# Kernel optimization log

Hardware: AMD Instinct MI355X
Metric: run time of the kernel (lower is better)

## Reference

```python
import jax, jax.numpy as jnp
import numpy as np

NX, NY, D, K = 20000, 50000, 64, 8
NUM_BATCHES = 2


def _knn_np(px, py, bx, by, k):
    # Batched exact kNN via chunked squared-distance + argpartition (mirrors torch_cluster.knn under no_grad).
    pp = (px * px).sum(1)
    idx = np.empty((py.shape[0], k), np.int32)
    chunk = 4096
    for s in range(0, py.shape[0], chunk):
        q = py[s:s + chunk]
        d = (q * q).sum(1)[:, None] + pp[None, :] - 2.0 * (q @ px.T)
        d = np.where(by[s:s + chunk, None] == bx[None, :], d, np.inf)
        idx[s:s + chunk] = np.argpartition(d, k, axis=1)[:, :k].astype(np.int32)
    return idx


def setup_inputs() -> dict:
    rng = np.random.default_rng(0)
    pos_x = (rng.random((NX, 3)) * 10.0).astype(np.float32)
    pos_y = (rng.random((NY, 3)) * 10.0).astype(np.float32)
    bx = np.repeat(np.arange(NUM_BATCHES), NX // NUM_BATCHES).astype(np.int32)
    by = np.repeat(np.arange(NUM_BATCHES), NY // NUM_BATCHES).astype(np.int32)
    x_idx = _knn_np(pos_x, pos_y, bx, by, K).reshape(-1)            # [NY*K]
    y_idx = np.repeat(np.arange(NY, dtype=np.int32), K)             # [NY*K]

    key = jax.random.key(0)
    ks = jax.random.split(key, 6)

    def lin(k, fi, fo):
        return jax.random.normal(k, (fi, fo), jnp.float32) / np.sqrt(fi).astype(np.float32)

    return {
        "x": jax.random.normal(ks[0], (NX, D), jnp.float32),
        "pos_x": jnp.asarray(pos_x),
        "pos_y": jnp.asarray(pos_y),
        "x_idx": jnp.asarray(x_idx),
        "y_idx": jnp.asarray(y_idx),
        # ResnetBlockFC 1: size_in=D+3, size_h=D, size_out=D (shortcut linear, no bias)
        "W0a": lin(ks[1], D + 3, D), "b0a": jnp.zeros((D,), jnp.float32),
        "W1a": lin(ks[2], D, D),     "b1a": jnp.zeros((D,), jnp.float32),
        "Wsa": lin(ks[3], D + 3, D),
        # ResnetBlockFC 2: size_in=size_h=size_out=D (identity shortcut)
        "W0b": lin(ks[4], D, D),     "b0b": jnp.zeros((D,), jnp.float32),
        "W1b": lin(ks[5], D, D),     "b1b": jnp.zeros((D,), jnp.float32),
    }


def reference(x, pos_x, pos_y, x_idx, y_idx, W0a, b0a, W1a, b1a, Wsa, W0b, b0b, W1b, b1b):
    # gather + positional diff (diff computed under no_grad in the original)
    diff = jax.lax.stop_gradient(pos_x[x_idx] - pos_y[y_idx])        # [E, 3]
    h = jnp.concatenate([x[x_idx], diff], axis=1)                    # [E, D+3]
    # ResnetBlockFC 1: out = shortcut(h) + fc1(relu(fc0(relu(h))))
    net = jax.nn.relu(h) @ W0a + b0a
    dx = jax.nn.relu(net) @ W1a + b1a
    h = h @ Wsa + dx                                                 # [E, D]
    # ResnetBlockFC 2 (identity shortcut)
    net = jax.nn.relu(h) @ W0b + b0b
    h = h + jax.nn.relu(net) @ W1b + b1b                             # [E, D]
    # scatter-max back to query points (every query has exactly K edges)
    out = jax.ops.segment_max(h, y_idx, num_segments=NY)             # [NY, D]
    return out
```

## Files before the change

### kernel.cpp

```cpp
#include <hip/hip_runtime.h>


typedef _Float16 f16x8 __attribute__((ext_vector_type(8)));
typedef float    f32x4 __attribute__((ext_vector_type(4)));

constexpr int NROWS   = 50000 * 8;
constexpr int NPAIRS  = NROWS / 32;
constexpr int NFRAG   = 48;
constexpr int TSTRIDE = 72;
constexpr int BW      = 8;

static __device__ __forceinline__ void xpose_relu(const f32x4* acc, const float* bb,
                                                  _Float16* tbuf, int q, int n0,
                                                  f16x8* af) {
    __threadfence_block();
#pragma unroll
    for (int t = 0; t < 4; ++t)
#pragma unroll
        for (int r = 0; r < 4; ++r) {
            float v = acc[t][r] + bb[t];
            tbuf[(q * 4 + r) * TSTRIDE + t * 16 + n0] = (_Float16)(v > 0.0f ? v : 0.0f);
        }
    __threadfence_block();
#pragma unroll
    for (int s = 0; s < 2; ++s)
        af[s] = *(const f16x8*)&tbuf[n0 * TSTRIDE + s * 32 + q * 8];
}

__global__ __launch_bounds__(512, 4)
void pointnet_fused(const float* __restrict__ x,
                    const float* __restrict__ pos_x,
                    const float* __restrict__ pos_y,
                    const int*   __restrict__ x_idx,
                    const float* __restrict__ W0a, const float* __restrict__ b0a,
                    const float* __restrict__ W1a, const float* __restrict__ b1a,
                    const float* __restrict__ Wsa,
                    const float* __restrict__ W0b, const float* __restrict__ b0b,
                    const float* __restrict__ W1b, const float* __restrict__ b1b,
                    float* __restrict__ out)
{
    __shared__ __align__(16) _Float16 bfrag[NFRAG * 64 * 8];
    __shared__ __align__(16) _Float16 trans[BW][16 * TSTRIDE];
    __shared__ float bias_lds[4 * 64];

    const int tid = threadIdx.x;

    for (int p = tid; p < NFRAG * 64; p += 512) {
        const int f = p >> 6;
        const int l = p & 63;
        const float* W; int krows, fl;
        if (f < 12)      { W = W0a; krows = 67; fl = f; }
        else if (f < 20) { W = W1a; krows = 64; fl = f - 12; }
        else if (f < 32) { W = Wsa; krows = 67; fl = f - 20; }
        else if (f < 40) { W = W0b; krows = 64; fl = f - 32; }
        else             { W = W1b; krows = 64; fl = f - 40; }
        const int s = fl >> 2, t = fl & 3;
        const int n = t * 16 + (l & 15);
        const int kbase = s * 32 + (l >> 4) * 8;
        f16x8 v;
#pragma unroll
        for (int j = 0; j < 8; ++j) {
            const int k = kbase + j;
            v[j] = (_Float16)((k < krows) ? W[k * 64 + n] : 0.0f);
        }
        *(f16x8*)&bfrag[p * 8] = v;
    }
    if (tid < 256) {
        const int L = tid >> 6, i = tid & 63;
        const float* b = (L == 0) ? b0a : (L == 1) ? b1a : (L == 2) ? b0b : b1b;
        bias_lds[tid] = b[i];
    }
    __syncthreads();

    const int lane = tid & 63;
    const int wv   = tid >> 6;
    const int n0   = lane & 15;
    const int q    = lane >> 4;

    _Float16* tbuf = trans[wv];
    const int gwave  = blockIdx.x * BW + wv;
    const int nwaves = gridDim.x * BW;

    for (int pr = gwave; pr < NPAIRS; pr += nwaves) {
        f16x8 hn[2][3];
#pragma unroll
        for (int u = 0; u < 2; ++u) {
            const int row = pr * 32 + u * 16 + n0;
            const int xi  = x_idx[row];
            const float* xp = x + (long)xi * 64;
#pragma unroll
            for (int s = 0; s < 2; ++s) {
                const float4* src = (const float4*)(xp + s * 32 + q * 8);
                float4 v0 = src[0], v1 = src[1];
                float vals[8] = {v0.x, v0.y, v0.z, v0.w, v1.x, v1.y, v1.z, v1.w};
#pragma unroll
                for (int j = 0; j < 8; ++j)
                    hn[u][s][j] = (_Float16)vals[j];
            }
            f16x8 z = {};
            hn[u][2] = z;
            if (q == 0) {
                const int yi = row >> 3;
#pragma unroll
                for (int j = 0; j < 3; ++j)
                    hn[u][2][j] = (_Float16)(pos_x[xi * 3 + j] - pos_y[yi * 3 + j]);
            }
        }

        f32x4 A2[2][4];
#pragma unroll
        for (int u = 0; u < 2; ++u)
#pragma unroll
            for (int t = 0; t < 4; ++t)
                A2[u][t] = (f32x4){0.f, 0.f, 0.f, 0.f};
#pragma unroll
        for (int s = 0; s < 3; ++s)
#pragma unroll
            for (int t = 0; t < 4; ++t) {
                f16x8 b = *(const f16x8*)&bfrag[((20 + s * 4 + t) * 64 + lane) * 8];
                A2[0][t] = __builtin_amdgcn_mfma_f32_16x16x32_f16(hn[0][s], b, A2[0][t], 0, 0, 0);
                A2[1][t] = __builtin_amdgcn_mfma_f32_16x16x32_f16(hn[1][s], b, A2[1][t], 0, 0, 0);
            }

#pragma unroll
        for (int u = 0; u < 2; ++u)
#pragma unroll
            for (int s = 0; s < 3; ++s)
#pragma unroll
                for (int j = 0; j < 8; ++j) {
                    _Float16 v = hn[u][s][j];
                    hn[u][s][j] = v > (_Float16)0 ? v : (_Float16)0;
                }

        f32x4 A1[2][4];
#pragma unroll
        for (int u = 0; u < 2; ++u)
#pragma unroll
            for (int t = 0; t < 4; ++t)
                A1[u][t] = (f32x4){0.f, 0.f, 0.f, 0.f};
#pragma unroll
        for (int s = 0; s < 3; ++s)
#pragma unroll
            for (int t = 0; t < 4; ++t) {
                f16x8 b = *(const f16x8*)&bfrag[((s * 4 + t) * 64 + lane) * 8];
                A1[0][t] = __builtin_amdgcn_mfma_f32_16x16x32_f16(hn[0][s], b, A1[0][t], 0, 0, 0);
                A1[1][t] = __builtin_amdgcn_mfma_f32_16x16x32_f16(hn[1][s], b, A1[1][t], 0, 0, 0);
            }

        float bb[4];
#pragma unroll
        for (int t = 0; t < 4; ++t) bb[t] = bias_lds[0 * 64 + t * 16 + n0];
        f16x8 a2[2][2];
        xpose_relu(A1[0], bb, tbuf, q, n0, a2[0]);
        xpose_relu(A1[1], bb, tbuf, q, n0, a2[1]);
#pragma unroll
        for (int s = 0; s < 2; ++s)
#pragma unroll
            for (int t = 0; t < 4; ++t) {
                f16x8 b = *(const f16x8*)&bfrag[((12 + s * 4 + t) * 64 + lane) * 8];
                A2[0][t] = __builtin_amdgcn_mfma_f32_16x16x32_f16(a2[0][s], b, A2[0][t], 0, 0, 0);
                A2[1][t] = __builtin_amdgcn_mfma_f32_16x16x32_f16(a2[1][s], b, A2[1][t], 0, 0, 0);
            }

#pragma unroll
        for (int t = 0; t < 4; ++t) bb[t] = bias_lds[1 * 64 + t * 16 + n0];
#pragma unroll
        for (int u = 0; u < 2; ++u)
#pragma unroll
            for (int t = 0; t < 4; ++t)
#pragma unroll
                for (int r = 0; r < 4; ++r)
                    A2[u][t][r] += bb[t];
        const float bz[4] = {0.f, 0.f, 0.f, 0.f};
        f16x8 a4[2][2];
        xpose_relu(A2[0], bz, tbuf, q, n0, a4[0]);
        xpose_relu(A2[1], bz, tbuf, q, n0, a4[1]);

        f32x4 A3[2][4];
#pragma unroll
        for (int u = 0; u < 2; ++u)
#pragma unroll
            for (int t = 0; t < 4; ++t)
                A3[u][t] = (f32x4){0.f, 0.f, 0.f, 0.f};
#pragma unroll
        for (int s = 0; s < 2; ++s)
#pragma unroll
            for (int t = 0; t < 4; ++t) {
                f16x8 b = *(const f16x8*)&bfrag[((32 + s * 4 + t) * 64 + lane) * 8];
                A3[0][t] = __builtin_amdgcn_mfma_f32_16x16x32_f16(a4[0][s], b, A3[0][t], 0, 0, 0);
                A3[1][t] = __builtin_amdgcn_mfma_f32_16x16x32_f16(a4[1][s], b, A3[1][t], 0, 0, 0);
            }

#pragma unroll
        for (int t = 0; t < 4; ++t) bb[t] = bias_lds[2 * 64 + t * 16 + n0];
        f16x8 a5[2][2];
        xpose_relu(A3[0], bb, tbuf, q, n0, a5[0]);
        xpose_relu(A3[1], bb, tbuf, q, n0, a5[1]);

#pragma unroll
        for (int t = 0; t < 4; ++t) bb[t] = bias_lds[3 * 64 + t * 16 + n0];
#pragma unroll
        for (int u = 0; u < 2; ++u)
#pragma unroll
            for (int t = 0; t < 4; ++t)
#pragma unroll
                for (int r = 0; r < 4; ++r)
                    A2[u][t][r] += bb[t];
#pragma unroll
        for (int s = 0; s < 2; ++s)
#pragma unroll
            for (int t = 0; t < 4; ++t) {
                f16x8 b = *(const f16x8*)&bfrag[((40 + s * 4 + t) * 64 + lane) * 8];
                A2[0][t] = __builtin_amdgcn_mfma_f32_16x16x32_f16(a5[0][s], b, A2[0][t], 0, 0, 0);
                A2[1][t] = __builtin_amdgcn_mfma_f32_16x16x32_f16(a5[1][s], b, A2[1][t], 0, 0, 0);
            }

#pragma unroll
        for (int u = 0; u < 2; ++u)
#pragma unroll
            for (int t = 0; t < 4; ++t) {
                float pm = fmaxf(fmaxf(A2[u][t][0], A2[u][t][1]),
                                 fmaxf(A2[u][t][2], A2[u][t][3]));
                pm = fmaxf(pm, __shfl_xor(pm, 16, 64));
                if ((q & 1) == 0) {
                    const int y = pr * 4 + u * 2 + (q >> 1);
                    out[(long)y * 64 + t * 16 + n0] = pm;
                }
            }
    }
}

extern "C" void kernel_launch(void* const* d_in, const int* in_sizes, int n_in,
                              void* d_out, int out_size, void* d_ws, size_t ws_size,
                              hipStream_t stream) {
    (void)in_sizes; (void)n_in; (void)d_ws; (void)ws_size; (void)out_size;
    pointnet_fused<<<512, 512, 0, stream>>>(
        (const float*)d_in[0],
        (const float*)d_in[1],
        (const float*)d_in[2],
        (const int*)  d_in[3],
        (const float*)d_in[5],  (const float*)d_in[6],
        (const float*)d_in[7],  (const float*)d_in[8],
        (const float*)d_in[9],
        (const float*)d_in[10], (const float*)d_in[11],
        (const float*)d_in[12], (const float*)d_in[13],
        (float*)d_out);
}
```

Baseline: 126.1 us.

## Precast x to fp16, precompute position diffs, and software-prefetch next gather

Adds two small pre-kernels that convert x to fp16 and compute the fp16 positional differences per edge into workspace. The fused kernel then gathers half-size rows and software-pipelines the loads, fetching the next pair's features and the index after that one while the current pair computes. This is meant to cut gather bandwidth and hide the latency of dependent index-then-row loads. The cost is two extra launches, a workspace round-trip for the diff buffer, and more live registers, which may hurt occupancy.

```diff
diff --git a/kernel.cpp b/kernel.cpp
--- a/kernel.cpp
+++ b/kernel.cpp
@@ -2,13 +2,40 @@
 
 
 typedef _Float16 f16x8 __attribute__((ext_vector_type(8)));
+typedef _Float16 f16x4 __attribute__((ext_vector_type(4)));
 typedef float    f32x4 __attribute__((ext_vector_type(4)));
 
+constexpr int NX      = 20000;
 constexpr int NROWS   = 50000 * 8;
 constexpr int NPAIRS  = NROWS / 32;
 constexpr int NFRAG   = 48;
 constexpr int TSTRIDE = 72;
 constexpr int BW      = 8;
+constexpr size_t X16_BYTES = (size_t)NX * 64 * 2;
+
+__global__ void prep_x(const float* __restrict__ x, _Float16* __restrict__ x16) {
+    const int i = blockIdx.x * blockDim.x + threadIdx.x;
+    if (i < NX * 16) {
+        float4 v = ((const float4*)x)[i];
+        f16x4 o = {(_Float16)v.x, (_Float16)v.y, (_Float16)v.z, (_Float16)v.w};
+        *(f16x4*)(x16 + (size_t)i * 4) = o;
+    }
+}
+
+__global__ void prep_diff(const int* __restrict__ x_idx,
+                          const float* __restrict__ px, const float* __restrict__ py,
+                          _Float16* __restrict__ d16) {
+    const int r = blockIdx.x * blockDim.x + threadIdx.x;
+    if (r < NROWS) {
+        const int xi = x_idx[r];
+        const int yi = r >> 3;
+        f16x4 o = {(_Float16)(px[xi * 3 + 0] - py[yi * 3 + 0]),
+                   (_Float16)(px[xi * 3 + 1] - py[yi * 3 + 1]),
+                   (_Float16)(px[xi * 3 + 2] - py[yi * 3 + 2]),
+                   (_Float16)0};
+        *(f16x4*)(d16 + (size_t)r * 4) = o;
+    }
+}
 
 static __device__ __forceinline__ void xpose_relu(const f32x4* acc, const float* bb,
                                                   _Float16* tbuf, int q, int n0,
@@ -28,9 +55,8 @@
 }
 
 __global__ __launch_bounds__(512, 4)
-void pointnet_fused(const float* __restrict__ x,
-                    const float* __restrict__ pos_x,
-                    const float* __restrict__ pos_y,
+void pointnet_fused(const _Float16* __restrict__ x16,
+                    const _Float16* __restrict__ d16,
                     const int*   __restrict__ x_idx,
                     const float* __restrict__ W0a, const float* __restrict__ b0a,
                     const float* __restrict__ W1a, const float* __restrict__ b1a,
@@ -80,31 +106,57 @@
     _Float16* tbuf = trans[wv];
     const int gwave  = blockIdx.x * BW + wv;
     const int nwaves = gridDim.x * BW;
+    const int last   = ((NPAIRS - 1 - gwave) / nwaves) * nwaves + gwave;
+
+    f16x8 cra[2][2];
+    f16x4 crd[2];
+    int   xin[2];
+
+#pragma unroll
+    for (int u = 0; u < 2; ++u) {
+        const int row = gwave * 32 + u * 16 + n0;
+        const int xi  = x_idx[row];
+        const _Float16* xp = x16 + (long)xi * 64 + q * 8;
+        cra[u][0] = *(const f16x8*)(xp);
+        cra[u][1] = *(const f16x8*)(xp + 32);
+        crd[u] = (f16x4){0, 0, 0, 0};
+        if (q == 0) crd[u] = *(const f16x4*)(d16 + (long)row * 4);
+    }
+    {
+        const int prn = (gwave + nwaves <= last) ? gwave + nwaves : last;
+#pragma unroll
+        for (int u = 0; u < 2; ++u)
+            xin[u] = x_idx[prn * 32 + u * 16 + n0];
+    }
 
     for (int pr = gwave; pr < NPAIRS; pr += nwaves) {
         f16x8 hn[2][3];
 #pragma unroll
         for (int u = 0; u < 2; ++u) {
-            const int row = pr * 32 + u * 16 + n0;
-            const int xi  = x_idx[row];
-            const float* xp = x + (long)xi * 64;
-#pragma unroll
-            for (int s = 0; s < 2; ++s) {
-                const float4* src = (const float4*)(xp + s * 32 + q * 8);
-                float4 v0 = src[0], v1 = src[1];
-                float vals[8] = {v0.x, v0.y, v0.z, v0.w, v1.x, v1.y, v1.z, v1.w};
-#pragma unroll
-                for (int j = 0; j < 8; ++j)
-                    hn[u][s][j] = (_Float16)vals[j];
-            }
+            hn[u][0] = cra[u][0];
+            hn[u][1] = cra[u][1];
             f16x8 z = {};
             hn[u][2] = z;
             if (q == 0) {
-                const int yi = row >> 3;
-#pragma unroll
-                for (int j = 0; j < 3; ++j)
-                    hn[u][2][j] = (_Float16)(pos_x[xi * 3 + j] - pos_y[yi * 3 + j]);
-            }
+                hn[u][2][0] = crd[u][0];
+                hn[u][2][1] = crd[u][1];
+                hn[u][2][2] = crd[u][2];
+            }
+        }
+
+        {
+            const int prn = (pr + nwaves <= last) ? pr + nwaves : last;
+#pragma unroll
+            for (int u = 0; u < 2; ++u) {
+                const _Float16* xp = x16 + (long)xin[u] * 64 + q * 8;
+                cra[u][0] = *(const f16x8*)(xp);
+                cra[u][1] = *(const f16x8*)(xp + 32);
+                if (q == 0) crd[u] = *(const f16x4*)(d16 + (long)(prn * 32 + u * 16 + n0) * 4);
+            }
+            const int prn2 = (prn + nwaves <= last) ? prn + nwaves : last;
+#pragma unroll
+            for (int u = 0; u < 2; ++u)
+                xin[u] = x_idx[prn2 * 32 + u * 16 + n0];
         }
 
         f32x4 A2[2][4];
@@ -233,11 +285,16 @@
 extern "C" void kernel_launch(void* const* d_in, const int* in_sizes, int n_in,
                               void* d_out, int out_size, void* d_ws, size_t ws_size,
                               hipStream_t stream) {
-    (void)in_sizes; (void)n_in; (void)d_ws; (void)ws_size; (void)out_size;
+    (void)in_sizes; (void)n_in; (void)ws_size; (void)out_size;
+    _Float16* x16 = (_Float16*)d_ws;
+    _Float16* d16 = (_Float16*)((char*)d_ws + X16_BYTES);
+
+    prep_x<<<(NX * 16 + 255) / 256, 256, 0, stream>>>((const float*)d_in[0], x16);
+    prep_diff<<<(NROWS + 255) / 256, 256, 0, stream>>>(
+        (const int*)d_in[3], (const float*)d_in[1], (const float*)d_in[2], d16);
+
     pointnet_fused<<<512, 512, 0, stream>>>(
-        (const float*)d_in[0],
-        (const float*)d_in[1],
-        (const float*)d_in[2],
+        x16, d16,
         (const int*)  d_in[3],
         (const float*)d_in[5],  (const float*)d_in[6],
         (const float*)d_in[7],  (const float*)d_in[8],
```

New measurement: 134.8 us. 1.07x slower.

## Pre-convert x to fp16 and process single 16-row tiles with more waves

Applied to the files above, without the earlier changes.

Adds a prep kernel that converts x to fp16 in workspace so the gather loads half the bytes per edge row. The main kernel now handles one 16-row tile per wave iteration instead of two, cutting register pressure. It raises the block to 12 waves with a higher occupancy hint to keep more waves resident. The cost is an extra kernel launch plus a full pass over x, and less instruction-level parallelism per wave.

```diff
diff --git a/kernel.cpp b/kernel.cpp
--- a/kernel.cpp
+++ b/kernel.cpp
@@ -2,13 +2,25 @@
 
 
 typedef _Float16 f16x8 __attribute__((ext_vector_type(8)));
+typedef _Float16 f16x4 __attribute__((ext_vector_type(4)));
 typedef float    f32x4 __attribute__((ext_vector_type(4)));
 
+constexpr int NX      = 20000;
 constexpr int NROWS   = 50000 * 8;
-constexpr int NPAIRS  = NROWS / 32;
+constexpr int NTILES  = NROWS / 16;
 constexpr int NFRAG   = 48;
 constexpr int TSTRIDE = 72;
-constexpr int BW      = 8;
+constexpr int BW      = 12;
+constexpr int BLOCK   = 64 * BW;
+
+__global__ void prep_x(const float* __restrict__ x, _Float16* __restrict__ x16) {
+    const int i = blockIdx.x * blockDim.x + threadIdx.x;
+    if (i < NX * 16) {
+        float4 v = ((const float4*)x)[i];
+        f16x4 o = {(_Float16)v.x, (_Float16)v.y, (_Float16)v.z, (_Float16)v.w};
+        *(f16x4*)(x16 + (size_t)i * 4) = o;
+    }
+}
 
 static __device__ __forceinline__ void xpose_relu(const f32x4* acc, const float* bb,
                                                   _Float16* tbuf, int q, int n0,
@@ -27,8 +39,8 @@
         af[s] = *(const f16x8*)&tbuf[n0 * TSTRIDE + s * 32 + q * 8];
 }
 
-__global__ __launch_bounds__(512, 4)
-void pointnet_fused(const float* __restrict__ x,
+__global__ __launch_bounds__(BLOCK, 6)
+void pointnet_fused(const _Float16* __restrict__ x16,
                     const float* __restrict__ pos_x,
                     const float* __restrict__ pos_y,
                     const int*   __restrict__ x_idx,
@@ -45,7 +57,7 @@
 
     const int tid = threadIdx.x;
 
-    for (int p = tid; p < NFRAG * 64; p += 512) {
+    for (int p = tid; p < NFRAG * 64; p += BLOCK) {
         const int f = p >> 6;
         const int l = p & 63;
         const float* W; int krows, fl;
@@ -81,161 +93,135 @@
     const int gwave  = blockIdx.x * BW + wv;
     const int nwaves = gridDim.x * BW;
 
-    for (int pr = gwave; pr < NPAIRS; pr += nwaves) {
-        f16x8 hn[2][3];
-#pragma unroll
-        for (int u = 0; u < 2; ++u) {
-            const int row = pr * 32 + u * 16 + n0;
-            const int xi  = x_idx[row];
-            const float* xp = x + (long)xi * 64;
-#pragma unroll
-            for (int s = 0; s < 2; ++s) {
-                const float4* src = (const float4*)(xp + s * 32 + q * 8);
-                float4 v0 = src[0], v1 = src[1];
-                float vals[8] = {v0.x, v0.y, v0.z, v0.w, v1.x, v1.y, v1.z, v1.w};
-#pragma unroll
-                for (int j = 0; j < 8; ++j)
-                    hn[u][s][j] = (_Float16)vals[j];
-            }
+    for (int tile = gwave; tile < NTILES; tile += nwaves) {
+        const int row = tile * 16 + n0;
+        const int xi  = x_idx[row];
+        const _Float16* xp = x16 + (long)xi * 64 + q * 8;
+        f16x8 hn[3];
+        hn[0] = *(const f16x8*)(xp);
+        hn[1] = *(const f16x8*)(xp + 32);
+        {
             f16x8 z = {};
-            hn[u][2] = z;
+            hn[2] = z;
             if (q == 0) {
                 const int yi = row >> 3;
 #pragma unroll
                 for (int j = 0; j < 3; ++j)
-                    hn[u][2][j] = (_Float16)(pos_x[xi * 3 + j] - pos_y[yi * 3 + j]);
-            }
-        }
-
-        f32x4 A2[2][4];
-#pragma unroll
-        for (int u = 0; u < 2; ++u)
-#pragma unroll
-            for (int t = 0; t < 4; ++t)
-                A2[u][t] = (f32x4){0.f, 0.f, 0.f, 0.f};
+                    hn[2][j] = (_Float16)(pos_x[xi * 3 + j] - pos_y[yi * 3 + j]);
+            }
+        }
+
+        f32x4 A2[4];
+#pragma unroll
+        for (int t = 0; t < 4; ++t)
+            A2[t] = (f32x4){0.f, 0.f, 0.f, 0.f};
 #pragma unroll
         for (int s = 0; s < 3; ++s)
 #pragma unroll
             for (int t = 0; t < 4; ++t) {
                 f16x8 b = *(const f16x8*)&bfrag[((20 + s * 4 + t) * 64 + lane) * 8];
-                A2[0][t] = __builtin_amdgcn_mfma_f32_16x16x32_f16(hn[0][s], b, A2[0][t], 0, 0, 0);
-                A2[1][t] = __builtin_amdgcn_mfma_f32_16x16x32_f16(hn[1][s], b, A2[1][t], 0, 0, 0);
-            }
-
-#pragma unroll
-        for (int u = 0; u < 2; ++u)
-#pragma unroll
-            for (int s = 0; s < 3; ++s)
-#pragma unroll
-                for (int j = 0; j < 8; ++j) {
-                    _Float16 v = hn[u][s][j];
-                    hn[u][s][j] = v > (_Float16)0 ? v : (_Float16)0;
-                }
-
-        f32x4 A1[2][4];
-#pragma unroll
-        for (int u = 0; u < 2; ++u)
-#pragma unroll
-            for (int t = 0; t < 4; ++t)
-                A1[u][t] = (f32x4){0.f, 0.f, 0.f, 0.f};
+                A2[t] = __builtin_amdgcn_mfma_f32_16x16x32_f16(hn[s], b, A2[t], 0, 0, 0);
+            }
+
 #pragma unroll
         for (int s = 0; s < 3; ++s)
 #pragma unroll
+            for (int j = 0; j < 8; ++j) {
+                _Float16 v = hn[s][j];
+                hn[s][j] = v > (_Float16)0 ? v : (_Float16)0;
+            }
+
+        f32x4 A1[4];
+#pragma unroll
+        for (int t = 0; t < 4; ++t)
+            A1[t] = (f32x4){0.f, 0.f, 0.f, 0.f};
+#pragma unroll
+        for (int s = 0; s < 3; ++s)
+#pragma unroll
             for (int t = 0; t < 4; ++t) {
                 f16x8 b = *(const f16x8*)&bfrag[((s * 4 + t) * 64 + lane) * 8];
-                A1[0][t] = __builtin_amdgcn_mfma_f32_16x16x32_f16(hn[0][s], b, A1[0][t], 0, 0, 0);
-                A1[1][t] = __builtin_amdgcn_mfma_f32_16x16x32_f16(hn[1][s], b, A1[1][t], 0, 0, 0);
+                A1[t] = __builtin_amdgcn_mfma_f32_16x16x32_f16(hn[s], b, A1[t], 0, 0, 0);
             }
 
         float bb[4];
 #pragma unroll
         for (int t = 0; t < 4; ++t) bb[t] = bias_lds[0 * 64 + t * 16 + n0];
-        f16x8 a2[2][2];
-        xpose_relu(A1[0], bb, tbuf, q, n0, a2[0]);
-        xpose_relu(A1[1], bb, tbuf, q, n0, a2[1]);
+        f16x8 a2f[2];
+        xpose_relu(A1, bb, tbuf, q, n0, a2f);
 #pragma unroll
         for (int s = 0; s < 2; ++s)
 #pragma unroll
             for (int t = 0; t < 4; ++t) {
                 f16x8 b = *(const f16x8*)&bfrag[((12 + s * 4 + t) * 64 + lane) * 8];
-                A2[0][t] = __builtin_amdgcn_mfma_f32_16x16x32_f16(a2[0][s], b, A2[0][t], 0, 0, 0);
-                A2[1][t] = __builtin_amdgcn_mfma_f32_16x16x32_f16(a2[1][s], b, A2[1][t], 0, 0, 0);
+                A2[t] = __builtin_amdgcn_mfma_f32_16x16x32_f16(a2f[s], b, A2[t], 0, 0, 0);
             }
 
 #pragma unroll
         for (int t = 0; t < 4; ++t) bb[t] = bias_lds[1 * 64 + t * 16 + n0];
 #pragma unroll
-        for (int u = 0; u < 2; ++u)
-#pragma unroll
-            for (int t = 0; t < 4; ++t)
-#pragma unroll
-                for (int r = 0; r < 4; ++r)
-                    A2[u][t][r] += bb[t];
+        for (int t = 0; t < 4; ++t)
+#pragma unroll
+            for (int r = 0; r < 4; ++r)
+                A2[t][r] += bb[t];
         const float bz[4] = {0.f, 0.f, 0.f, 0.f};
-        f16x8 a4[2][2];
-        xpose_relu(A2[0], bz, tbuf, q, n0, a4[0]);
-        xpose_relu(A2[1], bz, tbuf, q, n0, a4[1]);
-
-        f32x4 A3[2][4];
-#pragma unroll
-        for (int u = 0; u < 2; ++u)
-#pragma unroll
-            for (int t = 0; t < 4; ++t)
-                A3[u][t] = (f32x4){0.f, 0.f, 0.f, 0.f};
+        f16x8 a4f[2];
+        xpose_relu(A2, bz, tbuf, q, n0, a4f);
+
+        f32x4 A3[4];
+#pragma unroll
+        for (int t = 0; t < 4; ++t)
+            A3[t] = (f32x4){0.f, 0.f, 0.f, 0.f};
 #pragma unroll
         for (int s = 0; s < 2; ++s)
 #pragma unroll
             for (int t = 0; t < 4; ++t) {
                 f16x8 b = *(const f16x8*)&bfrag[((32 + s * 4 + t) * 64 + lane) * 8];
-                A3[0][t] = __builtin_amdgcn_mfma_f32_16x16x32_f16(a4[0][s], b, A3[0][t], 0, 0, 0);
-                A3[1][t] = __builtin_amdgcn_mfma_f32_16x16x32_f16(a4[1][s], b, A3[1][t], 0, 0, 0);
+                A3[t] = __builtin_amdgcn_mfma_f32_16x16x32_f16(a4f[s], b, A3[t], 0, 0, 0);
             }
 
 #pragma unroll
         for (int t = 0; t < 4; ++t) bb[t] = bias_lds[2 * 64 + t * 16 + n0];
-        f16x8 a5[2][2];
-        xpose_relu(A3[0], bb, tbuf, q, n0, a5[0]);
-        xpose_relu(A3[1], bb, tbuf, q, n0, a5[1]);
+        f16x8 a5f[2];
+        xpose_relu(A3, bb, tbuf, q, n0, a5f);
 
 #pragma unroll
         for (int t = 0; t < 4; ++t) bb[t] = bias_lds[3 * 64 + t * 16 + n0];
 #pragma unroll
-        for (int u = 0; u < 2; ++u)
-#pragma unroll
-            for (int t = 0; t < 4; ++t)
-#pragma unroll
-                for (int r = 0; r < 4; ++r)
-                    A2[u][t][r] += bb[t];
+        for (int t = 0; t < 4; ++t)
+#pragma unroll
+            for (int r = 0; r < 4; ++r)
+                A2[t][r] += bb[t];
 #pragma unroll
         for (int s = 0; s < 2; ++s)
 #pragma unroll
             for (int t = 0; t < 4; ++t) {
                 f16x8 b = *(const f16x8*)&bfrag[((40 + s * 4 + t) * 64 + lane) * 8];
-                A2[0][t] = __builtin_amdgcn_mfma_f32_16x16x32_f16(a5[0][s], b, A2[0][t], 0, 0, 0);
-                A2[1][t] = __builtin_amdgcn_mfma_f32_16x16x32_f16(a5[1][s], b, A2[1][t], 0, 0, 0);
-            }
-
-#pragma unroll
-        for (int u = 0; u < 2; ++u)
-#pragma unroll
-            for (int t = 0; t < 4; ++t) {
-                float pm = fmaxf(fmaxf(A2[u][t][0], A2[u][t][1]),
-                                 fmaxf(A2[u][t][2], A2[u][t][3]));
-                pm = fmaxf(pm, __shfl_xor(pm, 16, 64));
-                if ((q & 1) == 0) {
-                    const int y = pr * 4 + u * 2 + (q >> 1);
-                    out[(long)y * 64 + t * 16 + n0] = pm;
-                }
-            }
+                A2[t] = __builtin_amdgcn_mfma_f32_16x16x32_f16(a5f[s], b, A2[t], 0, 0, 0);
+            }
+
+#pragma unroll
+        for (int t = 0; t < 4; ++t) {
+            float pm = fmaxf(fmaxf(A2[t][0], A2[t][1]),
+                             fmaxf(A2[t][2], A2[t][3]));
+            pm = fmaxf(pm, __shfl_xor(pm, 16, 64));
+            if ((q & 1) == 0) {
+                const int y = tile * 2 + (q >> 1);
+                out[(long)y * 64 + t * 16 + n0] = pm;
+            }
+        }
     }
 }
 
 extern "C" void kernel_launch(void* const* d_in, const int* in_sizes, int n_in,
                               void* d_out, int out_size, void* d_ws, size_t ws_size,
                               hipStream_t stream) {
-    (void)in_sizes; (void)n_in; (void)d_ws; (void)ws_size; (void)out_size;
-    pointnet_fused<<<512, 512, 0, stream>>>(
-        (const float*)d_in[0],
+    (void)in_sizes; (void)n_in; (void)ws_size; (void)out_size;
+    _Float16* x16 = (_Float16*)d_ws;
+
+    prep_x<<<(NX * 16 + 255) / 256, 256, 0, stream>>>((const float*)d_in[0], x16);
+
+    pointnet_fused<<<512, BLOCK, 0, stream>>>(
+        x16,
         (const float*)d_in[1],
         (const float*)d_in[2],
         (const int*)  d_in[3],
```

New measurement: 126.5 us. Within noise of the previous version (+0.3%).
